# Kernel tuning notes

Hardware: AMD Instinct MI355X
Metric: run time of the kernel (lower is better)

## Reference

```python
import jax, jax.numpy as jnp
import numpy as np

B = 8192
ITEM_NUM = 10000


def setup_inputs() -> dict:
    key = jax.random.key(0)
    k1, k2, k3, k4, k5, k6 = jax.random.split(key, 6)
    hidden_states = jax.random.normal(k1, (B, ITEM_NUM), dtype=jnp.float32)
    targetQs_s = jax.random.normal(k2, (B, ITEM_NUM), dtype=jnp.float32)
    rewards = jax.random.uniform(k3, (B,), dtype=jnp.float32)
    actions = jax.random.randint(k4, (B,), 0, ITEM_NUM)
    is_done = jnp.zeros((B,), dtype=bool)
    discount = jnp.ones((), dtype=jnp.float32) * 0.99
    # fc = nn.Linear(item_num, 1): weight [1, item_num], bias [1]
    bound = 1.0 / np.sqrt(ITEM_NUM)
    W = jax.random.uniform(k5, (1, ITEM_NUM), minval=-bound, maxval=bound, dtype=jnp.float32)
    b = jax.random.uniform(k6, (1,), minval=-bound, maxval=bound, dtype=jnp.float32)
    return {
        "hidden_states": hidden_states,
        "actions": actions,
        "rewards": rewards,
        "discount": discount,
        "targetQs_s": targetQs_s,
        "is_done": is_done,
        "W": W,
        "b": b,
    }


def reference(hidden_states, actions, rewards, discount, targetQs_s, is_done, W, b):
    # Batched equivalent of the per-sample loop:
    # q_i = relu(fc(state_i)); nq_i = relu(fc(next_state_i))
    # loss_i = |reward_i + discount * nq_i - q_i| for non-done samples
    q = jax.nn.relu(jnp.einsum('bi,oi->bo', hidden_states, W) + b)[:, 0]   # [B]
    nq = jax.nn.relu(jnp.einsum('bi,oi->bo', targetQs_s, W) + b)[:, 0]     # [B]
    per_sample = jnp.abs(rewards + discount * nq - q)                      # [B]
    total = jnp.sum(jnp.where(is_done, jnp.float32(0.0), per_sample))
    return total / hidden_states.shape[0]
```

## Files before the change

### kernel.cpp

```cpp
#include <hip/hip_runtime.h>

#define ROWS 8192
#define COLS 10000
#define COLS4 (COLS / 4)
#define BLK 256
#define WAVES_PER_BLK (BLK / 64)

typedef float vf4 __attribute__((ext_vector_type(4)));

__device__ __forceinline__ float dot4(vf4 a, vf4 b) {
    return a.x * b.x + a.y * b.y + a.z * b.z + a.w * b.w;
}

__global__ __launch_bounds__(BLK) void qloss_rows_kernel(
    const float* __restrict__ hidden,
    const float* __restrict__ target,
    const float* __restrict__ rewards,
    const float* __restrict__ discount,
    const unsigned char* __restrict__ is_done,
    const float* __restrict__ W,
    const float* __restrict__ bias,
    float* __restrict__ partial)
{
    const int lane = threadIdx.x & 63;
    const int wid  = threadIdx.x >> 6;
    const int row  = blockIdx.x * WAVES_PER_BLK + wid;

    const vf4* __restrict__ h4 = (const vf4*)(hidden + (size_t)row * COLS);
    const vf4* __restrict__ t4 = (const vf4*)(target + (size_t)row * COLS);
    const vf4* __restrict__ w4 = (const vf4*)W;

    float ah0 = 0.f, ah1 = 0.f, at0 = 0.f, at1 = 0.f;
    int j = lane;
    for (; j + 64 < COLS4; j += 128) {
        vf4 w0 = w4[j];
        vf4 w1 = w4[j + 64];
        vf4 h0 = __builtin_nontemporal_load(&h4[j]);
        vf4 h1 = __builtin_nontemporal_load(&h4[j + 64]);
        vf4 t0 = __builtin_nontemporal_load(&t4[j]);
        vf4 t1 = __builtin_nontemporal_load(&t4[j + 64]);
        ah0 += dot4(h0, w0);
        ah1 += dot4(h1, w1);
        at0 += dot4(t0, w0);
        at1 += dot4(t1, w1);
    }
    if (j < COLS4) {
        vf4 w0 = w4[j];
        vf4 h0 = __builtin_nontemporal_load(&h4[j]);
        vf4 t0 = __builtin_nontemporal_load(&t4[j]);
        ah0 += dot4(h0, w0);
        at0 += dot4(t0, w0);
    }

    float ah = ah0 + ah1;
    float at = at0 + at1;

    #pragma unroll
    for (int off = 32; off > 0; off >>= 1) {
        ah += __shfl_down(ah, off, 64);
        at += __shfl_down(at, off, 64);
    }

    if (lane == 0) {
        float b  = bias[0];
        float q  = fmaxf(ah + b, 0.f);
        float nq = fmaxf(at + b, 0.f);
        float loss = fabsf(rewards[row] + discount[0] * nq - q);
        partial[row] = is_done[row] ? 0.f : loss;
    }
}

__global__ __launch_bounds__(BLK) void qloss_reduce_kernel(
    const float* __restrict__ partial,
    float* __restrict__ out)
{
    float s = 0.f;
    for (int i = threadIdx.x; i < ROWS; i += BLK) s += partial[i];

    #pragma unroll
    for (int off = 32; off > 0; off >>= 1) s += __shfl_down(s, off, 64);

    __shared__ float sm[BLK / 64];
    const int lane = threadIdx.x & 63;
    const int wid  = threadIdx.x >> 6;
    if (lane == 0) sm[wid] = s;
    __syncthreads();

    if (threadIdx.x == 0) {
        float total = sm[0] + sm[1] + sm[2] + sm[3];
        out[0] = total / (float)ROWS;
    }
}

extern "C" void kernel_launch(void* const* d_in, const int* in_sizes, int n_in,
                              void* d_out, int out_size, void* d_ws, size_t ws_size,
                              hipStream_t stream) {
    const float*         hidden   = (const float*)d_in[0];
    const float*         rewards  = (const float*)d_in[2];
    const float*         discount = (const float*)d_in[3];
    const float*         target   = (const float*)d_in[4];
    const unsigned char* is_done  = (const unsigned char*)d_in[5];
    const float*         W        = (const float*)d_in[6];
    const float*         b        = (const float*)d_in[7];
    float*               out      = (float*)d_out;
    float*               partial  = (float*)d_ws;

    qloss_rows_kernel<<<ROWS / WAVES_PER_BLK, BLK, 0, stream>>>(
        hidden, target, rewards, discount, is_done, W, b, partial);
    qloss_reduce_kernel<<<1, BLK, 0, stream>>>(partial, out);
}
```

Baseline: 597.6 us.

## Assign one row per block with fully unrolled column loop and LDS reduction

Changes the row kernel from one wave per row to a whole 256-thread block per row, launching one block per row. The column loop becomes a fixed 4-iteration unrolled loop plus explicit tail steps, and per-wave partial dot products are combined through shared memory before the loss is computed. The aim is more memory parallelism per row and contiguous block-wide access, at the cost of a block-level barrier and extra reduction work per row.

Measured after the change: 588.0 us. Within noise of the previous version (-1.6%).

```diff
diff --git a/kernel.cpp b/kernel.cpp
--- a/kernel.cpp
+++ b/kernel.cpp
@@ -4,7 +4,6 @@
 #define COLS 10000
 #define COLS4 (COLS / 4)
 #define BLK 256
-#define WAVES_PER_BLK (BLK / 64)
 
 typedef float vf4 __attribute__((ext_vector_type(4)));
 
@@ -22,34 +21,43 @@
     const float* __restrict__ bias,
     float* __restrict__ partial)
 {
-    const int lane = threadIdx.x & 63;
-    const int wid  = threadIdx.x >> 6;
-    const int row  = blockIdx.x * WAVES_PER_BLK + wid;
+    const int tid  = threadIdx.x;
+    const int lane = tid & 63;
+    const int wid  = tid >> 6;
+    const int row  = blockIdx.x;
 
     const vf4* __restrict__ h4 = (const vf4*)(hidden + (size_t)row * COLS);
     const vf4* __restrict__ t4 = (const vf4*)(target + (size_t)row * COLS);
     const vf4* __restrict__ w4 = (const vf4*)W;
 
     float ah0 = 0.f, ah1 = 0.f, at0 = 0.f, at1 = 0.f;
-    int j = lane;
-    for (; j + 64 < COLS4; j += 128) {
+    int j = tid;
+    for (int k = 0; k < 4; ++k, j += 512) {
         vf4 w0 = w4[j];
-        vf4 w1 = w4[j + 64];
+        vf4 w1 = w4[j + 256];
         vf4 h0 = __builtin_nontemporal_load(&h4[j]);
-        vf4 h1 = __builtin_nontemporal_load(&h4[j + 64]);
+        vf4 h1 = __builtin_nontemporal_load(&h4[j + 256]);
         vf4 t0 = __builtin_nontemporal_load(&t4[j]);
-        vf4 t1 = __builtin_nontemporal_load(&t4[j + 64]);
+        vf4 t1 = __builtin_nontemporal_load(&t4[j + 256]);
         ah0 += dot4(h0, w0);
         ah1 += dot4(h1, w1);
         at0 += dot4(t0, w0);
         at1 += dot4(t1, w1);
     }
-    if (j < COLS4) {
+    {
         vf4 w0 = w4[j];
         vf4 h0 = __builtin_nontemporal_load(&h4[j]);
         vf4 t0 = __builtin_nontemporal_load(&t4[j]);
         ah0 += dot4(h0, w0);
         at0 += dot4(t0, w0);
+    }
+    if (tid < COLS4 - 2304) {
+        int j2 = 2304 + tid;
+        vf4 w1 = w4[j2];
+        vf4 h1 = __builtin_nontemporal_load(&h4[j2]);
+        vf4 t1 = __builtin_nontemporal_load(&t4[j2]);
+        ah1 += dot4(h1, w1);
+        at1 += dot4(t1, w1);
     }
 
     float ah = ah0 + ah1;
@@ -61,10 +69,17 @@
         at += __shfl_down(at, off, 64);
     }
 
-    if (lane == 0) {
+    __shared__ float smh[BLK / 64];
+    __shared__ float smt[BLK / 64];
+    if (lane == 0) { smh[wid] = ah; smt[wid] = at; }
+    __syncthreads();
+
+    if (tid == 0) {
+        float AH = smh[0] + smh[1] + smh[2] + smh[3];
+        float AT = smt[0] + smt[1] + smt[2] + smt[3];
         float b  = bias[0];
-        float q  = fmaxf(ah + b, 0.f);
-        float nq = fmaxf(at + b, 0.f);
+        float q  = fmaxf(AH + b, 0.f);
+        float nq = fmaxf(AT + b, 0.f);
         float loss = fabsf(rewards[row] + discount[0] * nq - q);
         partial[row] = is_done[row] ? 0.f : loss;
     }
@@ -105,7 +120,7 @@
     float*               out      = (float*)d_out;
     float*               partial  = (float*)d_ws;
 
-    qloss_rows_kernel<<<ROWS / WAVES_PER_BLK, BLK, 0, stream>>>(
+    qloss_rows_kernel<<<ROWS, BLK, 0, stream>>>(
         hidden, target, rewards, discount, is_done, W, b, partial);
     qloss_reduce_kernel<<<1, BLK, 0, stream>>>(partial, out);
 }
```
